# Performance work log

Measured on AMD Instinct MI355X. Metric: run time of the kernel, lower is better.

Reference implementation:

```python
import jax, jax.numpy as jnp
import numpy as np

# --- architecture constants (match init_kwargs) ---
SLEN = 104
PTILE = 8
STEP = 2
N_BANDS = 2
MAX_DET = 2
N_SRC_PARAMS = 2
ENC_C = 20
ENC_HIDDEN = 256
# dim_out_all = 0.5*D*(D+1)*(4+2*n_source_params) + 1 + D  (probs over n_sources + per-count loc/flux mean+logvar)
DIM_OUT = int(0.5 * MAX_DET * (MAX_DET + 1) * (4 + 2 * N_SRC_PARAMS)) + 1 + MAX_DET  # 27


def _p(key, shape, scale=0.02):
    return scale * jax.random.normal(key, shape, dtype=jnp.float32)


def setup_inputs() -> dict:
    key = jax.random.key(0)
    ks = jax.random.split(key, 14)
    flat_in = ENC_C * PTILE * PTILE  # 20*8*8 = 1280
    return {
        "images": jax.random.normal(ks[0], (32, N_BANDS, SLEN, SLEN), dtype=jnp.float32),
        "conv1_w": _p(ks[1], (ENC_C, N_BANDS, 3, 3)),
        "conv1_b": _p(ks[2], (ENC_C,)),
        "conv2_w": _p(ks[3], (ENC_C, ENC_C, 3, 3)),
        "conv2_b": _p(ks[4], (ENC_C,)),
        "fc1_w": _p(ks[5], (ENC_HIDDEN, flat_in)),
        "fc1_b": _p(ks[6], (ENC_HIDDEN,)),
        "fc2_w": _p(ks[7], (ENC_HIDDEN, ENC_HIDDEN)),
        "fc2_b": _p(ks[8], (ENC_HIDDEN,)),
        "fc3_w": _p(ks[9], (ENC_HIDDEN, ENC_HIDDEN)),
        "fc3_b": _p(ks[10], (ENC_HIDDEN,)),
        "fcf_w": _p(ks[11], (DIM_OUT, ENC_HIDDEN)),
        "fcf_b": _p(ks[12], (DIM_OUT,)),
    }


def _tile_images(images):
    # torch tile_images: (B, C, slen, slen) -> (B * n_ptiles, C, P, P), tiles row-major over (x, y)
    B, C = images.shape[0], images.shape[1]
    patches = jax.lax.conv_general_dilated_patches(
        images, filter_shape=(PTILE, PTILE), window_strides=(STEP, STEP), padding="VALID"
    )  # (B, C*P*P, Hn, Wn) with feature dim ordered (C, P, P)
    Hn, Wn = patches.shape[2], patches.shape[3]
    p = patches.reshape(B, C, PTILE, PTILE, Hn, Wn)
    p = p.transpose(0, 4, 5, 1, 2, 3)  # (B, Hn, Wn, C, P, P)
    return p.reshape(B * Hn * Wn, C, PTILE, PTILE)


def _conv(x, w, b):
    y = jax.lax.conv_general_dilated(
        x, w, window_strides=(1, 1), padding="SAME",
        dimension_numbers=("NCHW", "OIHW", "NCHW"),
    )
    return y + b[None, :, None, None]


def reference(images, conv1_w, conv1_b, conv2_w, conv2_b,
              fc1_w, fc1_b, fc2_w, fc2_b, fc3_w, fc3_b, fcf_w, fcf_b):
    ptiles = _tile_images(images)                       # (B*nT, C, P, P)
    h = jax.nn.relu(_conv(ptiles, conv1_w, conv1_b))    # (B*nT, 20, P, P)
    h = jax.nn.relu(_conv(h, conv2_w, conv2_b))
    h = h.reshape(h.shape[0], -1)                       # Flatten -> (B*nT, 1280)
    h = jax.nn.relu(h @ fc1_w.T + fc1_b)
    h = jax.nn.relu(h @ fc2_w.T + fc2_b)
    h = jax.nn.relu(h @ fc3_w.T + fc3_b)
    return h @ fcf_w.T + fcf_b                          # (B*nT, dim_out_all)
```

## Files before the change

### kernel.cpp

```cpp
#include <hip/hip_runtime.h>
#include <hip/hip_bf16.h>

#define NPATCH 76832
#define NBLK   601
#define K1     1280

typedef __attribute__((ext_vector_type(8))) short  short8;
typedef __attribute__((ext_vector_type(4))) float  floatx4;

__device__ __forceinline__ unsigned short f2b(float f) {
    unsigned int u = __builtin_bit_cast(unsigned int, f);
    u += 0x7FFFu + ((u >> 16) & 1u);
    return (unsigned short)(u >> 16);
}
__device__ __forceinline__ unsigned int pk2(float a, float b) {
    __hip_bfloat162 h = __float22bfloat162_rn(make_float2(a, b));
    unsigned int u;
    __builtin_memcpy(&u, &h, 4);
    return u;
}

__device__ __forceinline__ void gload_lds16(const unsigned short* g, unsigned short* l) {
    __builtin_amdgcn_global_load_lds(
        (__attribute__((address_space(1))) void*)g,
        (__attribute__((address_space(3))) void*)l,
        16, 0, 0);
}

__device__ __host__ __forceinline__ int swz8(int row, int i) {
    return (((row & 1) * 4 + i) ^ ((row >> 1) & 7));
}

__global__ void prep(const float* __restrict__ f1w, const float* __restrict__ f2w,
                     const float* __restrict__ f3w, const float* __restrict__ c1w,
                     const float* __restrict__ c2w, const float* __restrict__ ffw,
                     unsigned short* __restrict__ W1F, unsigned short* __restrict__ W2F,
                     unsigned short* __restrict__ W3F, unsigned short* __restrict__ W1T,
                     unsigned short* __restrict__ W2T, unsigned short* __restrict__ WfF) {
    int i = blockIdx.x * 256 + threadIdx.x;
    if (i < 327680) {
        int o = i / 1280, k = i - o * 1280;
        int dst = ((k >> 5) * 16 + (o >> 6) * 4 + ((o >> 4) & 3)) * 512
                + (((k >> 3) & 3) * 16 + (o & 15)) * 8 + (k & 7);
        W1F[dst] = f2b(f1w[i]);
        return;
    }
    i -= 327680;
    if (i < 65536) {
        int o = i >> 8, k = i & 255;
        int dst = ((k >> 5) * 16 + (o >> 6) * 4 + ((o >> 4) & 3)) * 512
                + (((k >> 3) & 3) * 16 + (o & 15)) * 8 + (k & 7);
        W2F[dst] = f2b(f2w[i]);
        return;
    }
    i -= 65536;
    if (i < 65536) {
        int o = i >> 8, k = i & 255;
        int dst = ((k >> 5) * 16 + (o >> 6) * 4 + ((o >> 4) & 3)) * 512
                + (((k >> 3) & 3) * 16 + (o & 15)) * 8 + (k & 7);
        W3F[dst] = f2b(f3w[i]);
        return;
    }
    i -= 65536;
    if (i < 1024) {
        int o = i >> 5, k = i & 31;
        unsigned short v = 0;
        if (o < 20 && k < 18) v = f2b(c1w[o * 18 + k]);
        W1T[(o >> 1) * 64 + swz8(o, k >> 3) * 8 + (k & 7)] = v;
        return;
    }
    i -= 1024;
    if (i < 9216) {
        int tap = i >> 10, rem = i & 1023, o = rem >> 5, c = rem & 31;
        unsigned short v = 0;
        if (o < 20 && c < 20) v = f2b(c2w[o * 180 + c * 9 + tap]);
        W2T[tap * 1024 + (o >> 1) * 64 + swz8(o, c >> 3) * 8 + (c & 7)] = v;
        return;
    }
    i -= 9216;
    if (i < 8192) {
        int o = i >> 8, k = i & 255;
        unsigned short v = (o < 27) ? f2b(ffw[o * 256 + k]) : (unsigned short)0;
        int dst = ((k >> 5) * 2 + (o >> 4)) * 512
                + (((k >> 3) & 3) * 16 + (o & 15)) * 8 + (k & 7);
        WfF[dst] = v;
    }
}

__global__ __launch_bounds__(256, 3) void conv_mfma(
    const float* __restrict__ img,
    const unsigned short* __restrict__ W1T, const float* __restrict__ b1,
    const unsigned short* __restrict__ W2T, const float* __restrict__ b2,
    unsigned short* __restrict__ X, int row0)
{
    __shared__ alignas(16) unsigned short s_buf[8 * 2048 + 64];
    __shared__ alignas(16) unsigned short s_w1t[1024];
    __shared__ alignas(16) unsigned short s_w2t[9216];
    __shared__ float s_b1[32], s_b2[32];
    constexpr int ZOFF = 8 * 2048;

    const int tid = threadIdx.x;
    for (int d = tid; d < 512; d += 256)  ((unsigned int*)s_w1t)[d] = ((const unsigned int*)W1T)[d];
    for (int d = tid; d < 4608; d += 256) ((unsigned int*)s_w2t)[d] = ((const unsigned int*)W2T)[d];
    if (tid < 32) {
        ((unsigned int*)&s_buf[ZOFF])[tid] = 0u;
        s_b1[tid] = (tid < 20) ? b1[tid] : 0.f;
        s_b2[tid] = (tid < 20) ? b2[tid] : 0.f;
    }

    const int q = tid >> 5, t = tid & 31;
    const int Pl = blockIdx.x * 8 + q;
    const int Pi = row0 + Pl;
    const bool valid = Pi < NPATCH;
    int b = 0, hi = 0, wi = 0;
    if (valid) { b = Pi / 2401; int rem = Pi - b * 2401; hi = rem / 49; wi = rem - hi * 49; }
    const int py = t >> 2, px0 = (t & 3) * 2;
    const float* ib = img + (long long)b * 21632 + (hi * 2) * 104 + (wi * 2);

    float win[2][3][4];
    #pragma unroll
    for (int c = 0; c < 2; ++c)
        #pragma unroll
        for (int dy = 0; dy < 3; ++dy) {
            int ny = py + dy - 1;
            int nyc = ny < 0 ? 0 : (ny > 7 ? 7 : ny);
            #pragma unroll
            for (int dxw = 0; dxw < 4; ++dxw) {
                int nx = px0 + dxw - 1;
                int nxc = nx < 0 ? 0 : (nx > 7 ? 7 : nx);
                win[c][dy][dxw] = ib[c * 10816 + nyc * 104 + nxc];
            }
        }

    #pragma unroll
    for (int j = 0; j < 2; ++j) {
        const int px = px0 + j, pl = py * 8 + px;
        float val[18];
        #pragma unroll
        for (int c = 0; c < 2; ++c)
            #pragma unroll
            for (int dy = 0; dy < 3; ++dy) {
                int ny = py + dy - 1;
                bool rok = valid && ((unsigned)ny < 8u);
                #pragma unroll
                for (int dx = 0; dx < 3; ++dx) {
                    int nx = px + dx - 1;
                    bool ok = rok && ((unsigned)nx < 8u);
                    val[c * 9 + dy * 3 + dx] = ok ? win[c][dy][dx + j] : 0.f;
                }
            }
        alignas(16) unsigned int au[16];
        #pragma unroll
        for (int i = 0; i < 9; ++i) au[i] = pk2(val[2 * i], val[2 * i + 1]);
        #pragma unroll
        for (int i = 9; i < 16; ++i) au[i] = 0u;
        unsigned short* base = &s_buf[q * 2048 + (pl >> 1) * 64];
        #pragma unroll
        for (int i = 0; i < 4; ++i)
            *(uint4*)&base[swz8(pl, i) * 8] = ((const uint4*)au)[i];
    }
    __syncthreads();

    const int wave = tid >> 6, lane = tid & 63;
    const int l15 = lane & 15, quad = lane >> 4;
    const int p0 = wave * 2;

    int boffB[2];
    #pragma unroll
    for (int i = 0; i < 2; ++i) {
        int oo = i * 16 + l15;
        boffB[i] = (oo >> 1) * 64 + swz8(oo, quad) * 8;
    }

    short8 a1f[2];
    #pragma unroll
    for (int mt = 0; mt < 2; ++mt) a1f[mt] = *(const short8*)&s_w1t[boffB[mt]];

    floatx4 acc1[2][2][4] = {};
    #pragma unroll
    for (int pp = 0; pp < 2; ++pp)
        #pragma unroll
        for (int nt = 0; nt < 4; ++nt) {
            int pix = nt * 16 + l15;
            short8 pf = *(const short8*)&s_buf[(p0 + pp) * 2048 + (pix >> 1) * 64 + swz8(pix, quad) * 8];
            #pragma unroll
            for (int mt = 0; mt < 2; ++mt)
                acc1[pp][mt][nt] = __builtin_amdgcn_mfma_f32_16x16x32_bf16(a1f[mt], pf, acc1[pp][mt][nt], 0, 0, 0);
        }

    float bv1[2][4];
    #pragma unroll
    for (int mt = 0; mt < 2; ++mt)
        #pragma unroll
        for (int r = 0; r < 4; ++r) bv1[mt][r] = s_b1[mt * 16 + quad * 4 + r];

    #pragma unroll
    for (int pp = 0; pp < 2; ++pp)
        #pragma unroll
        for (int mt = 0; mt < 2; ++mt)
            #pragma unroll
            for (int nt = 0; nt < 4; ++nt) {
                floatx4 v = acc1[pp][mt][nt];
                uint2 w;
                w.x = pk2(fmaxf(v[0] + bv1[mt][0], 0.f), fmaxf(v[1] + bv1[mt][1], 0.f));
                w.y = pk2(fmaxf(v[2] + bv1[mt][2], 0.f), fmaxf(v[3] + bv1[mt][3], 0.f));
                int pix = nt * 16 + l15;
                int off = (p0 + pp) * 2048 + (pix >> 1) * 64
                        + swz8(pix, mt * 2 + (quad >> 1)) * 8 + (quad & 1) * 4;
                *(uint2*)&s_buf[off] = w;
            }

    int syv[4], pxv[4];
    #pragma unroll
    for (int mt = 0; mt < 4; ++mt) { int p = mt * 16 + l15; syv[mt] = p >> 3; pxv[mt] = p & 7; }

    floatx4 acc2[2][4][2] = {};
    #pragma unroll 1
    for (int dy = 0; dy < 3; ++dy) {
        int sy[4]; bool okY[4];
        #pragma unroll
        for (int mt = 0; mt < 4; ++mt) {
            sy[mt] = syv[mt] + dy - 1;
            okY[mt] = (unsigned)sy[mt] < 8u;
        }
        #pragma unroll
        for (int dx = 0; dx < 3; ++dx) {
            const int tap = dy * 3 + dx;
            short8 bf0 = *(const short8*)&s_w2t[tap * 1024 + boffB[0]];
            short8 bf1 = *(const short8*)&s_w2t[tap * 1024 + boffB[1]];
            #pragma unroll
            for (int mt = 0; mt < 4; ++mt) {
                int sx = pxv[mt] + dx - 1;
                bool ok = okY[mt] & ((unsigned)sx < 8u);
                int ps = sy[mt] * 8 + sx;
                int offl = (ps >> 1) * 64 + swz8(ps, quad) * 8;
                #pragma unroll
                for (int pp = 0; pp < 2; ++pp) {
                    int off = ok ? ((p0 + pp) * 2048 + offl) : (ZOFF + quad * 8);
                    short8 af = *(const short8*)&s_buf[off];
                    acc2[pp][mt][0] = __builtin_amdgcn_mfma_f32_16x16x32_bf16(af, bf0, acc2[pp][mt][0], 0, 0, 0);
                    acc2[pp][mt][1] = __builtin_amdgcn_mfma_f32_16x16x32_bf16(af, bf1, acc2[pp][mt][1], 0, 0, 0);
                }
            }
        }
    }

    #pragma unroll
    for (int pp = 0; pp < 2; ++pp) {
        unsigned short* xrow = X + (long long)(blockIdx.x * 8 + p0 + pp) * K1;
        #pragma unroll
        for (int nt = 0; nt < 2; ++nt) {
            const int col = nt * 16 + l15;
            if (col < 20) {
                const float bv = s_b2[col];
                #pragma unroll
                for (int mt = 0; mt < 4; ++mt) {
                    floatx4 v = acc2[pp][mt][nt];
                    uint2 w;
                    w.x = pk2(fmaxf(v[0] + bv, 0.f), fmaxf(v[1] + bv, 0.f));
                    w.y = pk2(fmaxf(v[2] + bv, 0.f), fmaxf(v[3] + bv, 0.f));
                    *(uint2*)&xrow[col * 64 + mt * 16 + quad * 4] = w;
                }
            }
        }
    }
}

__global__ __launch_bounds__(256, 3) void fc_all(
    const unsigned short* __restrict__ X,
    const unsigned short* __restrict__ W1F, const unsigned short* __restrict__ W2F,
    const unsigned short* __restrict__ W3F, const unsigned short* __restrict__ WfF,
    const float* __restrict__ b1, const float* __restrict__ b2,
    const float* __restrict__ b3, const float* __restrict__ bf_,
    float* __restrict__ out, int row0)
{
    __shared__ alignas(16) unsigned short s_a[64 * 128];
    __shared__ alignas(16) unsigned short s_h[64 * 256];

    const int tid = threadIdx.x;
    const int m0 = blockIdx.x * 64;
    const int wave = tid >> 6, lane = tid & 63;
    const int l15 = lane & 15, quad = lane >> 4;

    floatx4 acc[4][4];
    #pragma unroll
    for (int mt = 0; mt < 4; ++mt)
        #pragma unroll
        for (int nt = 0; nt < 4; ++nt) acc[mt][nt] = floatx4{0.f, 0.f, 0.f, 0.f};

    #pragma unroll 1
    for (int kt = 0; kt < 1280; kt += 128) {
        #pragma unroll
        for (int i = 0; i < 4; ++i) {
            int g = i * 256 + tid;
            int row = g >> 4, pos = g & 15;
            int cc = (pos & 8) | ((pos & 7) ^ (row & 7));
            gload_lds16(X + (long long)(m0 + row) * 1280 + kt + cc * 8,
                        &s_a[i * 2048 + wave * 512]);
        }
        __syncthreads();
        #pragma unroll
        for (int kh = 0; kh < 4; ++kh) {
            const int khg = (kt >> 5) + kh;
            short8 af[4], bf[4];
            #pragma unroll
            for (int mt = 0; mt < 4; ++mt)
                af[mt] = *(const short8*)(W1F + (khg * 16 + wave * 4 + mt) * 512 + lane * 8);
            #pragma unroll
            for (int nt = 0; nt < 4; ++nt) {
                int row = nt * 16 + l15;
                int c = kh * 4 + quad;
                int pos = (c & 8) | ((c & 7) ^ (row & 7));
                bf[nt] = *(const short8*)&s_a[row * 128 + pos * 8];
            }
            #pragma unroll
            for (int mt = 0; mt < 4; ++mt)
                #pragma unroll
                for (int nt = 0; nt < 4; ++nt)
                    acc[mt][nt] = __builtin_amdgcn_mfma_f32_16x16x32_bf16(af[mt], bf[nt], acc[mt][nt], 0, 0, 0);
        }
        __syncthreads();
    }
    #pragma unroll
    for (int mt = 0; mt < 4; ++mt) {
        int obase = wave * 64 + mt * 16 + quad * 4;
        float v0 = b1[obase], v1 = b1[obase + 1], v2 = b1[obase + 2], v3 = b1[obase + 3];
        int clow = mt * 2 + (quad >> 1), sub = (quad & 1) * 4;
        #pragma unroll
        for (int nt = 0; nt < 4; ++nt) {
            int row = nt * 16 + l15;
            int pos = wave * 8 + (clow ^ (row & 7));
            floatx4 v = acc[mt][nt];
            uint2 w;
            w.x = pk2(fmaxf(v[0] + v0, 0.f), fmaxf(v[1] + v1, 0.f));
            w.y = pk2(fmaxf(v[2] + v2, 0.f), fmaxf(v[3] + v3, 0.f));
            *(uint2*)&s_h[row * 256 + pos * 8 + sub] = w;
        }
    }
    __syncthreads();

    #pragma unroll 1
    for (int layer = 0; layer < 2; ++layer) {
        const unsigned short* Wp = (layer == 0) ? W2F : W3F;
        const float* bp = (layer == 0) ? b2 : b3;

        #pragma unroll
        for (int mt = 0; mt < 4; ++mt)
            #pragma unroll
            for (int nt = 0; nt < 4; ++nt) acc[mt][nt] = floatx4{0.f, 0.f, 0.f, 0.f};

        #pragma unroll
        for (int it = 0; it < 8; ++it) {
            short8 af[4], bf[4];
            #pragma unroll
            for (int mt = 0; mt < 4; ++mt)
                af[mt] = *(const short8*)(Wp + (it * 16 + wave * 4 + mt) * 512 + lane * 8);
            int chi = it >> 1, clo4 = (it & 1) * 4 + quad;
            #pragma unroll
            for (int nt = 0; nt < 4; ++nt) {
                int row = nt * 16 + l15;
                bf[nt] = *(const short8*)&s_h[row * 256 + (chi * 8 + (clo4 ^ (row & 7))) * 8];
            }
            #pragma unroll
            for (int mt = 0; mt < 4; ++mt)
                #pragma unroll
                for (int nt = 0; nt < 4; ++nt)
                    acc[mt][nt] = __builtin_amdgcn_mfma_f32_16x16x32_bf16(af[mt], bf[nt], acc[mt][nt], 0, 0, 0);
        }
        __syncthreads();
        #pragma unroll
        for (int mt = 0; mt < 4; ++mt) {
            int obase = wave * 64 + mt * 16 + quad * 4;
            float v0 = bp[obase], v1 = bp[obase + 1], v2 = bp[obase + 2], v3 = bp[obase + 3];
            int clow = mt * 2 + (quad >> 1), sub = (quad & 1) * 4;
            #pragma unroll
            for (int nt = 0; nt < 4; ++nt) {
                int row = nt * 16 + l15;
                int pos = wave * 8 + (clow ^ (row & 7));
                floatx4 v = acc[mt][nt];
                uint2 w;
                w.x = pk2(fmaxf(v[0] + v0, 0.f), fmaxf(v[1] + v1, 0.f));
                w.y = pk2(fmaxf(v[2] + v2, 0.f), fmaxf(v[3] + v3, 0.f));
                *(uint2*)&s_h[row * 256 + pos * 8 + sub] = w;
            }
        }
        __syncthreads();
    }

    floatx4 accf[2] = {};
    const int myrow = wave * 16 + l15;
    #pragma unroll
    for (int w8 = 0; w8 < 8; ++w8) {
        int chi = w8 >> 1, clo = (w8 & 1) * 4 + quad;
        short8 bfr = *(const short8*)&s_h[myrow * 256 + (chi * 8 + (clo ^ (myrow & 7))) * 8];
        #pragma unroll
        for (int mt = 0; mt < 2; ++mt) {
            short8 afr = *(const short8*)(WfF + (w8 * 2 + mt) * 512 + lane * 8);
            accf[mt] = __builtin_amdgcn_mfma_f32_16x16x32_bf16(afr, bfr, accf[mt], 0, 0, 0);
        }
    }
    const int grow = row0 + m0 + myrow;
    if (grow < NPATCH) {
        #pragma unroll
        for (int mt = 0; mt < 2; ++mt) {
            #pragma unroll
            for (int r = 0; r < 4; ++r) {
                int o = mt * 16 + quad * 4 + r;
                if (o < 27)
                    out[(long long)grow * 27 + o] = accf[mt][r] + bf_[o];
            }
        }
    }
}

extern "C" void kernel_launch(void* const* d_in, const int* in_sizes, int n_in,
                              void* d_out, int out_size, void* d_ws, size_t ws_size,
                              hipStream_t stream) {
    const float* images = (const float*)d_in[0];
    const float* c1w = (const float*)d_in[1];
    const float* c1b = (const float*)d_in[2];
    const float* c2w = (const float*)d_in[3];
    const float* c2b = (const float*)d_in[4];
    const float* f1w = (const float*)d_in[5];
    const float* f1b = (const float*)d_in[6];
    const float* f2w = (const float*)d_in[7];
    const float* f2b_ = (const float*)d_in[8];
    const float* f3w = (const float*)d_in[9];
    const float* f3b = (const float*)d_in[10];
    const float* ffw = (const float*)d_in[11];
    const float* ffb = (const float*)d_in[12];

    const long long W1_E = 327680, W2_E = 65536, W3_E = 65536;
    const long long W1T_E = 1024, W2T_E = 9216, WF_E = 8192;
    const long long WB = (W1_E + W2_E + W3_E + W1T_E + W2T_E + WF_E) * 2;
    char* ws = (char*)d_ws;
    unsigned short* W1F = (unsigned short*)ws;
    unsigned short* W2F = W1F + W1_E;
    unsigned short* W3F = W2F + W2_E;
    unsigned short* W1T = W3F + W3_E;
    unsigned short* W2T = W1T + W1T_E;
    unsigned short* WfF = W2T + W2T_E;
    unsigned short* X   = (unsigned short*)(ws + WB);

    long long avail = (long long)ws_size - WB - 256;
    int nb_max = (int)(avail / 327680LL);
    if (nb_max < 1) nb_max = 1;
    if (nb_max > NBLK) nb_max = NBLK;
    int nchunks = (NBLK + nb_max - 1) / nb_max;
    int nb_even = (NBLK + nchunks - 1) / nchunks;

    prep<<<1864, 256, 0, stream>>>(f1w, f2w, f3w, c1w, c2w, ffw, W1F, W2F, W3F, W1T, W2T, WfF);

    for (int b0 = 0; b0 < NBLK; b0 += nb_even) {
        int nb = NBLK - b0; if (nb > nb_even) nb = nb_even;
        int row0 = b0 * 128;
        int rows = nb * 128;

        conv_mfma<<<rows / 8, 256, 0, stream>>>(images, W1T, c1b, W2T, c2b, X, row0);
        fc_all<<<rows / 64, 256, 0, stream>>>(X, W1F, W2F, W3F, WfF,
                                              f1b, f2b_, f3b, ffb, (float*)d_out, row0);
    }
}
```

Baseline: 327.1 us.

## Store conv output in MFMA fragment layout and double-buffer FC1 input staging

Result: slower. 403.7 us (+23.4%).

```diff
diff --git a/kernel.cpp b/kernel.cpp
--- a/kernel.cpp
+++ b/kernel.cpp
@@ -93,19 +93,18 @@
     const unsigned short* __restrict__ W2T, const float* __restrict__ b2,
     unsigned short* __restrict__ X, int row0)
 {
-    __shared__ alignas(16) unsigned short s_buf[8 * 2048 + 64];
+    __shared__ alignas(16) unsigned short s_buf[8 * 2080];
     __shared__ alignas(16) unsigned short s_w1t[1024];
     __shared__ alignas(16) unsigned short s_w2t[9216];
     __shared__ float s_b1[32], s_b2[32];
-    constexpr int ZOFF = 8 * 2048;
 
     const int tid = threadIdx.x;
     for (int d = tid; d < 512; d += 256)  ((unsigned int*)s_w1t)[d] = ((const unsigned int*)W1T)[d];
     for (int d = tid; d < 4608; d += 256) ((unsigned int*)s_w2t)[d] = ((const unsigned int*)W2T)[d];
     if (tid < 32) {
-        ((unsigned int*)&s_buf[ZOFF])[tid] = 0u;
         s_b1[tid] = (tid < 20) ? b1[tid] : 0.f;
         s_b2[tid] = (tid < 20) ? b2[tid] : 0.f;
+        *(uint4*)&s_buf[(tid >> 2) * 2080 + 2048 + (tid & 3) * 8] = make_uint4(0u, 0u, 0u, 0u);
     }
 
     const int q = tid >> 5, t = tid & 31;
@@ -154,16 +153,19 @@
         for (int i = 0; i < 9; ++i) au[i] = pk2(val[2 * i], val[2 * i + 1]);
         #pragma unroll
         for (int i = 9; i < 16; ++i) au[i] = 0u;
-        unsigned short* base = &s_buf[q * 2048 + (pl >> 1) * 64];
-        #pragma unroll
-        for (int i = 0; i < 4; ++i)
-            *(uint4*)&base[swz8(pl, i) * 8] = ((const uint4*)au)[i];
+        unsigned short* base = &s_buf[q * 2080 + (pl >> 1) * 64];
+        #pragma unroll
+        for (int i = 0; i < 4; ++i) {
+            int ii = i ^ ((t >> 3) & 3);
+            *(uint4*)&base[swz8(pl, ii) * 8] = ((const uint4*)au)[ii];
+        }
     }
     __syncthreads();
 
     const int wave = tid >> 6, lane = tid & 63;
     const int l15 = lane & 15, quad = lane >> 4;
     const int p0 = wave * 2;
+    const int pb0 = p0 * 2080, pb1 = pb0 + 2080;
 
     int boffB[2];
     #pragma unroll
@@ -182,7 +184,7 @@
         #pragma unroll
         for (int nt = 0; nt < 4; ++nt) {
             int pix = nt * 16 + l15;
-            short8 pf = *(const short8*)&s_buf[(p0 + pp) * 2048 + (pix >> 1) * 64 + swz8(pix, quad) * 8];
+            short8 pf = *(const short8*)&s_buf[(p0 + pp) * 2080 + (pix >> 1) * 64 + swz8(pix, quad) * 8];
             #pragma unroll
             for (int mt = 0; mt < 2; ++mt)
                 acc1[pp][mt][nt] = __builtin_amdgcn_mfma_f32_16x16x32_bf16(a1f[mt], pf, acc1[pp][mt][nt], 0, 0, 0);
@@ -205,14 +207,15 @@
                 w.x = pk2(fmaxf(v[0] + bv1[mt][0], 0.f), fmaxf(v[1] + bv1[mt][1], 0.f));
                 w.y = pk2(fmaxf(v[2] + bv1[mt][2], 0.f), fmaxf(v[3] + bv1[mt][3], 0.f));
                 int pix = nt * 16 + l15;
-                int off = (p0 + pp) * 2048 + (pix >> 1) * 64
+                int off = (p0 + pp) * 2080 + (pix >> 1) * 64
                         + swz8(pix, mt * 2 + (quad >> 1)) * 8 + (quad & 1) * 4;
                 *(uint2*)&s_buf[off] = w;
             }
 
-    int syv[4], pxv[4];
-    #pragma unroll
-    for (int mt = 0; mt < 4; ++mt) { int p = mt * 16 + l15; syv[mt] = p >> 3; pxv[mt] = p & 7; }
+    const int pxl = l15 & 7;
+    int syv[4];
+    #pragma unroll
+    for (int mt = 0; mt < 4; ++mt) syv[mt] = mt * 2 + (l15 >> 3);
 
     floatx4 acc2[2][4][2] = {};
     #pragma unroll 1
@@ -226,28 +229,32 @@
         #pragma unroll
         for (int dx = 0; dx < 3; ++dx) {
             const int tap = dy * 3 + dx;
+            const int sx = pxl + dx - 1;
+            const bool okX = (unsigned)sx < 8u;
+            const int sl4q = ((sx & 1) << 2) | quad;
             short8 bf0 = *(const short8*)&s_w2t[tap * 1024 + boffB[0]];
             short8 bf1 = *(const short8*)&s_w2t[tap * 1024 + boffB[1]];
             #pragma unroll
             for (int mt = 0; mt < 4; ++mt) {
-                int sx = pxv[mt] + dx - 1;
-                bool ok = okY[mt] & ((unsigned)sx < 8u);
-                int ps = sy[mt] * 8 + sx;
-                int offl = (ps >> 1) * 64 + swz8(ps, quad) * 8;
-                #pragma unroll
-                for (int pp = 0; pp < 2; ++pp) {
-                    int off = ok ? ((p0 + pp) * 2048 + offl) : (ZOFF + quad * 8);
-                    short8 af = *(const short8*)&s_buf[off];
-                    acc2[pp][mt][0] = __builtin_amdgcn_mfma_f32_16x16x32_bf16(af, bf0, acc2[pp][mt][0], 0, 0, 0);
-                    acc2[pp][mt][1] = __builtin_amdgcn_mfma_f32_16x16x32_bf16(af, bf1, acc2[pp][mt][1], 0, 0, 0);
-                }
+                const bool ok = okX & okY[mt];
+                const int ps = sy[mt] * 8 + sx;
+                const int psh = ps >> 1;
+                const int offl = psh * 64 + ((sl4q ^ (psh & 7)) << 3);
+                const int offz = ok ? offl : (2048 + quad * 8);
+                short8 af0 = *(const short8*)&s_buf[pb0 + offz];
+                short8 af1 = *(const short8*)&s_buf[pb1 + offz];
+                acc2[0][mt][0] = __builtin_amdgcn_mfma_f32_16x16x32_bf16(af0, bf0, acc2[0][mt][0], 0, 0, 0);
+                acc2[0][mt][1] = __builtin_amdgcn_mfma_f32_16x16x32_bf16(af0, bf1, acc2[0][mt][1], 0, 0, 0);
+                acc2[1][mt][0] = __builtin_amdgcn_mfma_f32_16x16x32_bf16(af1, bf0, acc2[1][mt][0], 0, 0, 0);
+                acc2[1][mt][1] = __builtin_amdgcn_mfma_f32_16x16x32_bf16(af1, bf1, acc2[1][mt][1], 0, 0, 0);
             }
         }
     }
 
     #pragma unroll
     for (int pp = 0; pp < 2; ++pp) {
-        unsigned short* xrow = X + (long long)(blockIdx.x * 8 + p0 + pp) * K1;
+        const int r_rel = blockIdx.x * 8 + p0 + pp;
+        const int rb = r_rel >> 4, rl = r_rel & 15;
         #pragma unroll
         for (int nt = 0; nt < 2; ++nt) {
             const int col = nt * 16 + l15;
@@ -259,14 +266,16 @@
                     uint2 w;
                     w.x = pk2(fmaxf(v[0] + bv, 0.f), fmaxf(v[1] + bv, 0.f));
                     w.y = pk2(fmaxf(v[2] + bv, 0.f), fmaxf(v[3] + bv, 0.f));
-                    *(uint2*)&xrow[col * 64 + mt * 16 + quad * 4] = w;
+                    long long idx = (long long)(rb * 40 + col * 2 + (mt >> 1)) * 512
+                                  + ((mt & 1) * 2 + (quad >> 1)) * 128 + rl * 8 + (quad & 1) * 4;
+                    *(uint2*)&X[idx] = w;
                 }
             }
         }
     }
 }
 
-__global__ __launch_bounds__(256, 3) void fc_all(
+__global__ __launch_bounds__(256, 4) void fc_all(
     const unsigned short* __restrict__ X,
     const unsigned short* __restrict__ W1F, const unsigned short* __restrict__ W2F,
     const unsigned short* __restrict__ W3F, const unsigned short* __restrict__ WfF,
@@ -274,8 +283,7 @@
     const float* __restrict__ b3, const float* __restrict__ bf_,
     float* __restrict__ out, int row0)
 {
-    __shared__ alignas(16) unsigned short s_a[64 * 128];
-    __shared__ alignas(16) unsigned short s_h[64 * 256];
+    __shared__ alignas(16) unsigned short s_mem[16384];
 
     const int tid = threadIdx.x;
     const int m0 = blockIdx.x * 64;
@@ -288,31 +296,31 @@
         #pragma unroll
         for (int nt = 0; nt < 4; ++nt) acc[mt][nt] = floatx4{0.f, 0.f, 0.f, 0.f};
 
-    #pragma unroll 1
-    for (int kt = 0; kt < 1280; kt += 128) {
-        #pragma unroll
-        for (int i = 0; i < 4; ++i) {
-            int g = i * 256 + tid;
-            int row = g >> 4, pos = g & 15;
-            int cc = (pos & 8) | ((pos & 7) ^ (row & 7));
-            gload_lds16(X + (long long)(m0 + row) * 1280 + kt + cc * 8,
-                        &s_a[i * 2048 + wave * 512]);
-        }
-        __syncthreads();
+    const unsigned short* xsrc = X + (long long)(((m0 >> 4) + wave) * 40) * 512 + lane * 8;
+    auto stage = [&](int buf, int c) {
+        unsigned short* dst = &s_mem[buf * 8192 + wave * 512];
+        const unsigned short* src = xsrc + (4 * c) * 512;
+        #pragma unroll
+        for (int i = 0; i < 4; ++i)
+            gload_lds16(src + i * 512, dst + i * 2048);
+    };
+
+    stage(0, 0);
+    __syncthreads();
+    #pragma unroll 2
+    for (int c = 0; c < 10; ++c) {
+        if (c < 9) stage((c + 1) & 1, c + 1);
+        const int bb = (c & 1) * 8192;
         #pragma unroll
         for (int kh = 0; kh < 4; ++kh) {
-            const int khg = (kt >> 5) + kh;
+            const int khg = 4 * c + kh;
             short8 af[4], bf[4];
             #pragma unroll
             for (int mt = 0; mt < 4; ++mt)
                 af[mt] = *(const short8*)(W1F + (khg * 16 + wave * 4 + mt) * 512 + lane * 8);
             #pragma unroll
-            for (int nt = 0; nt < 4; ++nt) {
-                int row = nt * 16 + l15;
-                int c = kh * 4 + quad;
-                int pos = (c & 8) | ((c & 7) ^ (row & 7));
-                bf[nt] = *(const short8*)&s_a[row * 128 + pos * 8];
-            }
+            for (int nt = 0; nt < 4; ++nt)
+                bf[nt] = *(const short8*)&s_mem[bb + (kh * 4 + nt) * 512 + lane * 8];
             #pragma unroll
             for (int mt = 0; mt < 4; ++mt)
                 #pragma unroll
@@ -321,20 +329,20 @@
         }
         __syncthreads();
     }
+
     #pragma unroll
     for (int mt = 0; mt < 4; ++mt) {
-        int obase = wave * 64 + mt * 16 + quad * 4;
-        float v0 = b1[obase], v1 = b1[obase + 1], v2 = b1[obase + 2], v3 = b1[obase + 3];
-        int clow = mt * 2 + (quad >> 1), sub = (quad & 1) * 4;
+        const int obase = wave * 64 + mt * 16 + quad * 4;
+        const float v0 = b1[obase], v1 = b1[obase + 1], v2 = b1[obase + 2], v3 = b1[obase + 3];
+        const int slot = (wave * 2 + (mt >> 1)) * 4;
+        const int qk = (mt & 1) * 2 + (quad >> 1);
         #pragma unroll
         for (int nt = 0; nt < 4; ++nt) {
-            int row = nt * 16 + l15;
-            int pos = wave * 8 + (clow ^ (row & 7));
             floatx4 v = acc[mt][nt];
             uint2 w;
             w.x = pk2(fmaxf(v[0] + v0, 0.f), fmaxf(v[1] + v1, 0.f));
             w.y = pk2(fmaxf(v[2] + v2, 0.f), fmaxf(v[3] + v3, 0.f));
-            *(uint2*)&s_h[row * 256 + pos * 8 + sub] = w;
+            *(uint2*)&s_mem[(slot + nt) * 512 + qk * 128 + l15 * 8 + (quad & 1) * 4] = w;
         }
     }
     __syncthreads();
@@ -355,12 +363,9 @@
             #pragma unroll
             for (int mt = 0; mt < 4; ++mt)
                 af[mt] = *(const short8*)(Wp + (it * 16 + wave * 4 + mt) * 512 + lane * 8);
-            int chi = it >> 1, clo4 = (it & 1) * 4 + quad;
-            #pragma unroll
-            for (int nt = 0; nt < 4; ++nt) {
-                int row = nt * 16 + l15;
-                bf[nt] = *(const short8*)&s_h[row * 256 + (chi * 8 + (clo4 ^ (row & 7))) * 8];
-            }
+            #pragma unroll
+            for (int nt = 0; nt < 4; ++nt)
+                bf[nt] = *(const short8*)&s_mem[(it * 4 + nt) * 512 + lane * 8];
             #pragma unroll
             for (int mt = 0; mt < 4; ++mt)
                 #pragma unroll
@@ -370,29 +375,27 @@
         __syncthreads();
         #pragma unroll
         for (int mt = 0; mt < 4; ++mt) {
-            int obase = wave * 64 + mt * 16 + quad * 4;
-            float v0 = bp[obase], v1 = bp[obase + 1], v2 = bp[obase + 2], v3 = bp[obase + 3];
-            int clow = mt * 2 + (quad >> 1), sub = (quad & 1) * 4;
+            const int obase = wave * 64 + mt * 16 + quad * 4;
+            const float v0 = bp[obase], v1 = bp[obase + 1], v2 = bp[obase + 2], v3 = bp[obase + 3];
+            const int slot = (wave * 2 + (mt >> 1)) * 4;
+            const int qk = (mt & 1) * 2 + (quad >> 1);
             #pragma unroll
             for (int nt = 0; nt < 4; ++nt) {
-                int row = nt * 16 + l15;
-                int pos = wave * 8 + (clow ^ (row & 7));
                 floatx4 v = acc[mt][nt];
                 uint2 w;
                 w.x = pk2(fmaxf(v[0] + v0, 0.f), fmaxf(v[1] + v1, 0.f));
                 w.y = pk2(fmaxf(v[2] + v2, 0.f), fmaxf(v[3] + v3, 0.f));
-                *(uint2*)&s_h[row * 256 + pos * 8 + sub] = w;
+                *(uint2*)&s_mem[(slot + nt) * 512 + qk * 128 + l15 * 8 + (quad & 1) * 4] = w;
             }
         }
         __syncthreads();
     }
 
-    floatx4 accf[2] = {};
+    floatx4 accf[2] = {floatx4{0.f, 0.f, 0.f, 0.f}, floatx4{0.f, 0.f, 0.f, 0.f}};
     const int myrow = wave * 16 + l15;
     #pragma unroll
     for (int w8 = 0; w8 < 8; ++w8) {
-        int chi = w8 >> 1, clo = (w8 & 1) * 4 + quad;
-        short8 bfr = *(const short8*)&s_h[myrow * 256 + (chi * 8 + (clo ^ (myrow & 7))) * 8];
+        short8 bfr = *(const short8*)&s_mem[(w8 * 4 + wave) * 512 + lane * 8];
         #pragma unroll
         for (int mt = 0; mt < 2; ++mt) {
             short8 afr = *(const short8*)(WfF + (w8 * 2 + mt) * 512 + lane * 8);
```
